# Kernel optimization log

Hardware: AMD Instinct MI355X
Metric: run time of the kernel (lower is better)

Reference implementation:

```python
import jax, jax.numpy as jnp
import numpy as np

EMB = 768
HEADS = 12
HEAD_DIM = EMB // HEADS
FF = 4 * EMB
EPS = 1e-5


def setup_inputs() -> dict:
    key = jax.random.key(0)
    ks = jax.random.split(key, 12)
    s = 0.02
    return {
        "x": jax.random.normal(ks[0], (4, 2048, EMB), dtype=jnp.float32),
        "ln1_scale": jnp.ones((EMB,), jnp.float32),
        "ln1_shift": jnp.zeros((EMB,), jnp.float32),
        # weights stored [in, out] (transpose of torch Linear layout)
        "wq": jax.random.normal(ks[1], (EMB, EMB), jnp.float32) * s,
        "wk": jax.random.normal(ks[2], (EMB, EMB), jnp.float32) * s,
        "wv": jax.random.normal(ks[3], (EMB, EMB), jnp.float32) * s,
        "wo": jax.random.normal(ks[4], (EMB, EMB), jnp.float32) * s,
        "bo": jnp.zeros((EMB,), jnp.float32),
        "ln2_scale": jnp.ones((EMB,), jnp.float32),
        "ln2_shift": jnp.zeros((EMB,), jnp.float32),
        "w1": jax.random.normal(ks[5], (EMB, FF), jnp.float32) * s,
        "b1": jnp.zeros((FF,), jnp.float32),
        "w2": jax.random.normal(ks[6], (FF, EMB), jnp.float32) * s,
        "b2": jnp.zeros((EMB,), jnp.float32),
    }


def _layernorm(x, scale, shift):
    mean = jnp.mean(x, axis=-1, keepdims=True)
    var = jnp.mean(jnp.square(x - mean), axis=-1, keepdims=True)  # unbiased=False
    return scale * (x - mean) / jnp.sqrt(var + EPS) + shift


def _gelu_tanh(x):
    c = jnp.sqrt(jnp.float32(2.0 / np.pi))
    return 0.5 * x * (1.0 + jnp.tanh(c * (x + 0.044715 * x * x * x)))


def _attention(x, wq, wk, wv, wo, bo):
    b, s, _ = x.shape
    q = (x @ wq).reshape(b, s, HEADS, HEAD_DIM).transpose(0, 2, 1, 3)
    k = (x @ wk).reshape(b, s, HEADS, HEAD_DIM).transpose(0, 2, 1, 3)
    v = (x @ wv).reshape(b, s, HEADS, HEAD_DIM).transpose(0, 2, 1, 3)
    scores = jnp.einsum("bhqd,bhkd->bhqk", q, k)  # [B,H,S,S]
    causal = jnp.tril(jnp.ones((s, s), dtype=bool))
    scores = jnp.where(causal, scores, -jnp.inf)
    weights = jax.nn.softmax(scores / jnp.sqrt(jnp.float32(HEAD_DIM)), axis=-1)
    ctx = jnp.einsum("bhqk,bhkd->bhqd", weights, v)
    ctx = ctx.transpose(0, 2, 1, 3).reshape(b, s, EMB)
    return ctx @ wo + bo


def reference(x, ln1_scale, ln1_shift, wq, wk, wv, wo, bo,
              ln2_scale, ln2_shift, w1, b1, w2, b2):
    # dropout rate is 0.0 (inference) -> identity
    x = x + _attention(_layernorm(x, ln1_scale, ln1_shift), wq, wk, wv, wo, bo)
    h = _layernorm(x, ln2_scale, ln2_shift)
    h = _gelu_tanh(h @ w1 + b1) @ w2 + b2
    return x + h
```

## Files before the change

kernel.cpp:

```cpp
#include <hip/hip_runtime.h>
#include <stdint.h>

#define EMB 768
#define SEQ 2048
#define BATCH 4
#define NHEADS 12
#define HDIM 64
#define FFDIM 3072
#define NTOK (BATCH*SEQ)
#define LNEPS 1e-5f
#define QSCALE 0.1803368801111137f

typedef __attribute__((ext_vector_type(8))) short bf16x8;
typedef __attribute__((ext_vector_type(4))) float f32x4;

__device__ __forceinline__ uint16_t f2bf(float f){
  union { float f; uint32_t u; } v; v.f = f;
  uint32_t r = v.u + 0x7fffu + ((v.u >> 16) & 1u);
  return (uint16_t)(r >> 16);
}
__device__ __forceinline__ uint32_t pk_rhu(float lo, float hi){
  union { float f; uint32_t u; } a, b; a.f = lo; b.f = hi;
  return __builtin_amdgcn_perm(b.u + 0x8000u, a.u + 0x8000u, 0x07060302u);
}

typedef __attribute__((address_space(3))) uint32_t lds32_t;
typedef __attribute__((address_space(1))) const uint32_t glb32_t;
__device__ __forceinline__ void gload16(const void* g, void* l){
  __builtin_amdgcn_global_load_lds((glb32_t*)(uintptr_t)g,
                                   (lds32_t*)(uintptr_t)l, 16, 0, 0);
}

struct TPtrs { const float* src[6]; uint16_t* dst[6]; };
__global__ __launch_bounds__(256) void transpose_all(TPtrs tp){
  int idx = blockIdx.x;
  int which, bx, by, K, N;
  if (idx < 2304){ which = idx/576; int l = idx - which*576; bx = l%24; by = l/24; K = 768;  N = 768;  }
  else if (idx < 4608){ which = 4; int l = idx-2304; bx = l%96; by = l/96; K = 768;  N = 3072; }
  else { which = 5; int l = idx-4608; bx = l%24; by = l/24; K = 3072; N = 768;  }
  const float* w = tp.src[which];
  uint16_t* wt   = tp.dst[which];
  __shared__ uint16_t tile[32][33];
  int n0 = bx*32, k0 = by*32;
  #pragma unroll
  for (int i=0;i<4;i++){
    int k = threadIdx.y + i*8;
    tile[k][threadIdx.x] = f2bf(w[(size_t)(k0+k)*N + n0 + threadIdx.x]);
  }
  __syncthreads();
  #pragma unroll
  for (int i=0;i<4;i++){
    int n = threadIdx.y + i*8;
    wt[(size_t)(n0+n)*K + k0 + threadIdx.x] = tile[threadIdx.x][n];
  }
}

__global__ __launch_bounds__(256) void ln_kernel(const float* __restrict__ x,
    const float* __restrict__ sc, const float* __restrict__ sh,
    uint16_t* __restrict__ out)
{
  int row = blockIdx.x*4 + (threadIdx.x>>6);
  int ln = threadIdx.x & 63;
  const float4* xr = (const float4*)(x + (size_t)row*EMB);
  float4 v0 = xr[ln], v1 = xr[64+ln], v2 = xr[128+ln];
  float s  = v0.x+v0.y+v0.z+v0.w + v1.x+v1.y+v1.z+v1.w + v2.x+v2.y+v2.z+v2.w;
  float s2 = v0.x*v0.x+v0.y*v0.y+v0.z*v0.z+v0.w*v0.w
           + v1.x*v1.x+v1.y*v1.y+v1.z*v1.z+v1.w*v1.w
           + v2.x*v2.x+v2.y*v2.y+v2.z*v2.z+v2.w*v2.w;
  #pragma unroll
  for (int off=1;off<64;off<<=1){ s += __shfl_xor(s,off); s2 += __shfl_xor(s2,off); }
  float mean = s*(1.f/768.f);
  float var  = s2*(1.f/768.f) - mean*mean;
  float rstd = rsqrtf(var + LNEPS);
  uint16_t* orow = out + (size_t)row*EMB;
  float4 vv[3] = {v0,v1,v2};
  #pragma unroll
  for (int i=0;i<3;i++){
    int c = (i*64+ln)*4;
    ushort4 o4;
    o4.x = f2bf((vv[i].x-mean)*rstd*sc[c+0] + sh[c+0]);
    o4.y = f2bf((vv[i].y-mean)*rstd*sc[c+1] + sh[c+1]);
    o4.z = f2bf((vv[i].z-mean)*rstd*sc[c+2] + sh[c+2]);
    o4.w = f2bf((vv[i].w-mean)*rstd*sc[c+3] + sh[c+3]);
    *(ushort4*)(orow + c) = o4;
  }
}

template<int MODE>
__global__ __launch_bounds__(256) void gemm_bt(const uint16_t* __restrict__ A,
    const uint16_t* __restrict__ Bt0,
    const float* __restrict__ bias,
    const float* __restrict__ resid,
    void* __restrict__ outp,
    uint16_t* __restrict__ vt_out,
    int N, int K, long bt_zstride, long out_zstride)
{
  __shared__ __align__(16) uint16_t As[128][32];
  __shared__ __align__(16) uint16_t Bs[128][32];
  const uint16_t* Bt = Bt0 + (size_t)blockIdx.z * bt_zstride;
  int tid = threadIdx.x;
  int wave = tid>>6, ln = tid&63, lane16 = ln&15, quad = ln>>4;
  int m0 = blockIdx.x*128, n0 = blockIdx.y*128;
  int wm = (wave>>1)*64, wn = (wave&1)*64;
  f32x4 zf = {0.f,0.f,0.f,0.f};
  f32x4 acc[4][4];
  #pragma unroll
  for (int i=0;i<4;i++)
    #pragma unroll
    for (int j=0;j<4;j++) acc[i][j]=zf;
  int ar = tid>>2;
  int ac = (tid&3)*8;
  const uint16_t* Arow0 = A  + (size_t)(m0+ar)*K    + ac;
  const uint16_t* Arow1 = A  + (size_t)(m0+ar+64)*K + ac;
  const uint16_t* Brow0 = Bt + (size_t)(n0+ar)*K    + ac;
  const uint16_t* Brow1 = Bt + (size_t)(n0+ar+64)*K + ac;
  char* lA = (char*)&As[0][0] + wave*1024;
  char* lB = (char*)&Bs[0][0] + wave*1024;
  for (int k0=0;k0<K;k0+=32){
    __syncthreads();
    gload16(Arow0 + k0, lA);
    gload16(Arow1 + k0, lA + 4096);
    gload16(Brow0 + k0, lB);
    gload16(Brow1 + k0, lB + 4096);
    __syncthreads();
    bf16x8 af[4], bfr[4];
    #pragma unroll
    for (int mi=0;mi<4;mi++) af[mi]  = *(const bf16x8*)&As[wm+mi*16+lane16][quad*8];
    #pragma unroll
    for (int ni=0;ni<4;ni++) bfr[ni] = *(const bf16x8*)&Bs[wn+ni*16+lane16][quad*8];
    #pragma unroll
    for (int mi=0;mi<4;mi++)
      #pragma unroll
      for (int ni=0;ni<4;ni++)
        acc[mi][ni] = __builtin_amdgcn_mfma_f32_16x16x32_bf16(af[mi], bfr[ni], acc[mi][ni], 0,0,0);
  }
  if (MODE==0 && blockIdx.z==2){
    #pragma unroll
    for (int mi=0;mi<4;mi++){
      int mrow0 = m0 + wm + mi*16 + quad*4;
      int bb = mrow0 >> 11, s = mrow0 & 2047;
      #pragma unroll
      for (int ni=0;ni<4;ni++){
        int ncol = n0 + wn + ni*16 + lane16;
        int hh = ncol >> 6, dd = ncol & 63;
        ushort4 o4 = { f2bf(acc[mi][ni][0]), f2bf(acc[mi][ni][1]),
                       f2bf(acc[mi][ni][2]), f2bf(acc[mi][ni][3]) };
        *(ushort4*)(vt_out + ((size_t)((bb*NHEADS+hh)*HDIM + dd))*SEQ + s) = o4;
      }
    }
    return;
  }
  float oscale = (MODE==0 && blockIdx.z==0) ? QSCALE : 1.0f;
  #pragma unroll
  for (int mi=0;mi<4;mi++){
    #pragma unroll
    for (int r=0;r<4;r++){
      int mrow = m0 + wm + mi*16 + quad*4 + r;
      #pragma unroll
      for (int ni=0;ni<4;ni++){
        int ncol = n0 + wn + ni*16 + lane16;
        float vv = acc[mi][ni][r];
        size_t idx = (size_t)mrow*N + ncol;
        if (MODE==0){
          ((uint16_t*)outp)[(size_t)blockIdx.z*out_zstride + idx] = f2bf(vv*oscale);
        } else if (MODE==1){
          ((float*)outp)[idx] = vv + bias[ncol] + resid[idx];
        } else if (MODE==2){
          float t = vv + bias[ncol];
          float u = 1.5957691216057308f*(t + 0.044715f*t*t*t);
          ((uint16_t*)outp)[idx] = f2bf(t / (1.f + __expf(-u)));
        } else {
          ((float*)outp)[idx] = vv + bias[ncol] + resid[idx];
        }
      }
    }
  }
}

__global__ __launch_bounds__(256, 3) void attn_kernel(const uint16_t* __restrict__ q,
    const uint16_t* __restrict__ k, const uint16_t* __restrict__ vt,
    uint16_t* __restrict__ ctx)
{
  __shared__ __align__(16) uint16_t Ks[2][8][64][8];
  __shared__ __align__(16) uint16_t Vs[2][8][64][8];
  const f32x4 zf = {0.f,0.f,0.f,0.f};
  int tid = threadIdx.x;
  int wave = tid>>6, ln = tid&63, l16 = ln&15, quad = ln>>4;
  int b = blockIdx.z, h = blockIdx.y;
  int p = blockIdx.x;
  size_t kgbase = ((size_t)(b*SEQ + ln))*EMB + h*HDIM;
  size_t vgbase = ((size_t)((b*NHEADS + h)*HDIM + ln))*SEQ;

  f32x4 o[4];
  float m_l, l_l;
  bf16x8 qf0, qf1;
  int q0w, myq;

  auto stage = [&](int buf, int kv0){
    #pragma unroll
    for (int i=0;i<2;i++){
      int c = wave + 4*i;
      gload16(k  + kgbase + (size_t)kv0*EMB + c*8, &Ks[buf][c][0][0]);
      gload16(vt + vgbase + kv0 + c*8,             &Vs[buf][c][0][0]);
    }
  };
  auto init_tile = [&](int tile){
    q0w = tile*64 + wave*16;
    myq = q0w + l16;
    const uint16_t* qrow = q + ((size_t)(b*SEQ + q0w + l16))*EMB + h*HDIM + quad*8;
    qf0 = *(const bf16x8*)(qrow);
    qf1 = *(const bf16x8*)(qrow + 32);
    o[0]=zf; o[1]=zf; o[2]=zf; o[3]=zf;
    m_l = -3.0e38f; l_l = 0.f;
  };
  auto writeout = [&](){
    float inv = 1.0f / l_l;
    uint16_t* crow = ctx + ((size_t)(b*SEQ + q0w + l16))*EMB + h*HDIM + quad*4;
    #pragma unroll
    for (int t=0; t<4; t++){
      ushort4 w4 = { f2bf(o[t][0]*inv), f2bf(o[t][1]*inv),
                     f2bf(o[t][2]*inv), f2bf(o[t][3]*inv) };
      *(ushort4*)(crow + t*16) = w4;
    }
  };
  auto compute = [&](int buf, int kv0, bool masked){
    bf16x8 kf[4][2], vf[2][4];
    #pragma unroll
    for (int f=0; f<4; f++){
      kf[f][0] = *(const bf16x8*)&Ks[buf][quad  ][f*16+l16][0];
      kf[f][1] = *(const bf16x8*)&Ks[buf][quad+4][f*16+l16][0];
    }
    #pragma unroll
    for (int t=0; t<4; t++){
      vf[0][t] = *(const bf16x8*)&Vs[buf][quad  ][t*16+l16][0];
      vf[1][t] = *(const bf16x8*)&Vs[buf][quad+4][t*16+l16][0];
    }
    f32x4 st[4];
    #pragma unroll
    for (int f=0; f<4; f++){
      st[f] = __builtin_amdgcn_mfma_f32_16x16x32_bf16(kf[f][0], qf0, zf, 0,0,0);
      st[f] = __builtin_amdgcn_mfma_f32_16x16x32_bf16(kf[f][1], qf1, st[f], 0,0,0);
    }
    if (masked){
      #pragma unroll
      for (int f=0; f<4; f++){
        int kvf = kv0 + f*16 + quad*4;
        #pragma unroll
        for (int r=0; r<4; r++)
          if (kvf + r > myq) st[f][r] = -1e30f;
      }
    }
    float cmax = -1e30f;
    #pragma unroll
    for (int f=0; f<4; f++)
      #pragma unroll
      for (int r=0; r<4; r++) cmax = fmaxf(cmax, st[f][r]);
    cmax = fmaxf(cmax, __shfl_xor(cmax,16));
    cmax = fmaxf(cmax, __shfl_xor(cmax,32));
    float mn = fmaxf(m_l, cmax);
    float alpha = __builtin_amdgcn_exp2f(m_l - mn);
    float rs = 0.f;
    #pragma unroll
    for (int f=0; f<4; f++)
      #pragma unroll
      for (int r=0; r<4; r++){
        st[f][r] = __builtin_amdgcn_exp2f(st[f][r] - mn);
        rs += st[f][r];
      }
    rs += __shfl_xor(rs,16); rs += __shfl_xor(rs,32);
    l_l = l_l*alpha + rs; m_l = mn;
    #pragma unroll
    for (int t=0; t<4; t++)
      #pragma unroll
      for (int r=0; r<4; r++) o[t][r] *= alpha;
    uint32_t dw[4][2];
    #pragma unroll
    for (int f=0; f<4; f++){
      dw[f][0] = pk_rhu(st[f][0], st[f][1]);
      dw[f][1] = pk_rhu(st[f][2], st[f][3]);
    }
    union { uint32_t u[4]; bf16x8 v; } pb[2];
    #pragma unroll
    for (int g=0; g<2; g++)
      #pragma unroll
      for (int j=0; j<4; j++){
        int src = 16*(2*(quad&1) + (j>>1)) + l16;
        uint32_t lo = (uint32_t)__shfl((int)dw[2*g  ][j&1], src, 64);
        uint32_t hi = (uint32_t)__shfl((int)dw[2*g+1][j&1], src, 64);
        pb[g].u[j] = (quad>>1) ? hi : lo;
      }
    #pragma unroll
    for (int t=0; t<4; t++){
      o[t] = __builtin_amdgcn_mfma_f32_16x16x32_bf16(vf[0][t], pb[0].v, o[t], 0,0,0);
      o[t] = __builtin_amdgcn_mfma_f32_16x16x32_bf16(vf[1][t], pb[1].v, o[t], 0,0,0);
    }
  };

  int n0 = p + 1, ntot = 33;
  init_tile(p);
  stage(0, 0);
  for (int s=0; s<ntot; s++){
    int sl = (s < n0) ? s : s - n0;
    int kv0 = sl*64;
    __syncthreads();
    if (s+1 < ntot){
      int sn = s+1;
      int snl = (sn < n0) ? sn : sn - n0;
      stage(sn&1, snl*64);
    }
    if (s == n0){ writeout(); init_tile(31 - p); }
    bool masked = (s == n0-1) || (s == ntot-1);
    compute(s&1, kv0, masked);
  }
  writeout();
}

extern "C" void kernel_launch(void* const* d_in, const int* in_sizes, int n_in,
                              void* d_out, int out_size, void* d_ws, size_t ws_size,
                              hipStream_t stream) {
  const float* x     = (const float*)d_in[0];
  const float* ln1_s = (const float*)d_in[1];
  const float* ln1_b = (const float*)d_in[2];
  const float* wq    = (const float*)d_in[3];
  const float* wk    = (const float*)d_in[4];
  const float* wv    = (const float*)d_in[5];
  const float* wo    = (const float*)d_in[6];
  const float* bo    = (const float*)d_in[7];
  const float* ln2_s = (const float*)d_in[8];
  const float* ln2_b = (const float*)d_in[9];
  const float* w1    = (const float*)d_in[10];
  const float* b1    = (const float*)d_in[11];
  const float* w2    = (const float*)d_in[12];
  const float* b2    = (const float*)d_in[13];

  uint16_t* wqkv_t = (uint16_t*)d_ws;
  uint16_t* wo_t   = wqkv_t + 3*EMB*EMB;
  uint16_t* w1_t   = wo_t   + EMB*EMB;
  uint16_t* w2_t   = w1_t   + (size_t)FFDIM*EMB;
  uint16_t* xn     = w2_t   + (size_t)EMB*FFDIM;
  uint16_t* qkv    = xn     + (size_t)NTOK*EMB;
  uint16_t* ctx    = qkv    + (size_t)3*NTOK*EMB;
  uint16_t* hff    = qkv;
  float*    x1     = (float*)(ctx + (size_t)NTOK*EMB);
  uint16_t* vt     = (uint16_t*)(x1 + (size_t)NTOK*EMB);

  TPtrs tp;
  tp.src[0]=wq; tp.src[1]=wk; tp.src[2]=wv; tp.src[3]=wo; tp.src[4]=w1; tp.src[5]=w2;
  tp.dst[0]=wqkv_t; tp.dst[1]=wqkv_t+EMB*EMB; tp.dst[2]=wqkv_t+2*EMB*EMB;
  tp.dst[3]=wo_t; tp.dst[4]=w1_t; tp.dst[5]=w2_t;
  transpose_all<<<6912, dim3(32,8), 0, stream>>>(tp);

  ln_kernel<<<NTOK/4, 256, 0, stream>>>(x, ln1_s, ln1_b, xn);
  gemm_bt<0><<<dim3(NTOK/128, EMB/128, 3), 256, 0, stream>>>(
      xn, wqkv_t, nullptr, nullptr, qkv, vt, EMB, EMB,
      (long)EMB*EMB, (long)NTOK*EMB);
  attn_kernel<<<dim3(16, NHEADS, BATCH), 256, 0, stream>>>(
      qkv, qkv + (size_t)NTOK*EMB, vt, ctx);
  gemm_bt<1><<<dim3(NTOK/128, EMB/128, 1), 256, 0, stream>>>(
      ctx, wo_t, bo, x, x1, nullptr, EMB, EMB, 0, 0);
  ln_kernel<<<NTOK/4, 256, 0, stream>>>(x1, ln2_s, ln2_b, xn);
  gemm_bt<2><<<dim3(NTOK/128, FFDIM/128, 1), 256, 0, stream>>>(
      xn, w1_t, b1, nullptr, hff, nullptr, FFDIM, EMB, 0, 0);
  gemm_bt<3><<<dim3(NTOK/128, EMB/128, 1), 256, 0, stream>>>(
      hff, w2_t, b2, x1, d_out, nullptr, EMB, FFDIM, 0, 0);
}
```

Measured before the change: 414.6 us.

## Double-buffer GEMM LDS tiles and use 64-row tiles for narrow-N GEMMs

The GEMM kernel gets two LDS buffers, so the next K-slice is fetched into one buffer while MFMAs run on the other. This removes one barrier per iteration and overlaps global-to-LDS loads with compute. A TM template parameter lets the N=768 output projection and FFN-down GEMMs use 64-row tiles, doubling their block count from 384 to 768 to fill the GPU better. Launch bounds now request 4 blocks per CU, which doubles LDS per block and may constrain registers.

```diff
diff --git a/kernel.cpp b/kernel.cpp
--- a/kernel.cpp
+++ b/kernel.cpp
@@ -86,8 +86,8 @@
   }
 }
 
-template<int MODE>
-__global__ __launch_bounds__(256) void gemm_bt(const uint16_t* __restrict__ A,
+template<int MODE, int TM>
+__global__ __launch_bounds__(256, 4) void gemm_bt(const uint16_t* __restrict__ A,
     const uint16_t* __restrict__ Bt0,
     const float* __restrict__ bias,
     const float* __restrict__ resid,
@@ -95,17 +95,18 @@
     uint16_t* __restrict__ vt_out,
     int N, int K, long bt_zstride, long out_zstride)
 {
-  __shared__ __align__(16) uint16_t As[128][32];
-  __shared__ __align__(16) uint16_t Bs[128][32];
+  constexpr int MI = TM/32;
+  __shared__ __align__(16) uint16_t As[2][TM][32];
+  __shared__ __align__(16) uint16_t Bs[2][128][32];
   const uint16_t* Bt = Bt0 + (size_t)blockIdx.z * bt_zstride;
   int tid = threadIdx.x;
   int wave = tid>>6, ln = tid&63, lane16 = ln&15, quad = ln>>4;
-  int m0 = blockIdx.x*128, n0 = blockIdx.y*128;
-  int wm = (wave>>1)*64, wn = (wave&1)*64;
+  int m0 = blockIdx.x*TM, n0 = blockIdx.y*128;
+  int wm = (wave>>1)*(MI*16), wn = (wave&1)*64;
   f32x4 zf = {0.f,0.f,0.f,0.f};
-  f32x4 acc[4][4];
-  #pragma unroll
-  for (int i=0;i<4;i++)
+  f32x4 acc[MI][4];
+  #pragma unroll
+  for (int i=0;i<MI;i++)
     #pragma unroll
     for (int j=0;j<4;j++) acc[i][j]=zf;
   int ar = tid>>2;
@@ -114,29 +115,36 @@
   const uint16_t* Arow1 = A  + (size_t)(m0+ar+64)*K + ac;
   const uint16_t* Brow0 = Bt + (size_t)(n0+ar)*K    + ac;
   const uint16_t* Brow1 = Bt + (size_t)(n0+ar+64)*K + ac;
-  char* lA = (char*)&As[0][0] + wave*1024;
-  char* lB = (char*)&Bs[0][0] + wave*1024;
-  for (int k0=0;k0<K;k0+=32){
-    __syncthreads();
+
+  auto stage = [&](int buf, int k0){
+    char* lA = (char*)&As[buf][0][0] + wave*1024;
+    char* lB = (char*)&Bs[buf][0][0] + wave*1024;
     gload16(Arow0 + k0, lA);
-    gload16(Arow1 + k0, lA + 4096);
+    if (TM==128) gload16(Arow1 + k0, lA + 4096);
     gload16(Brow0 + k0, lB);
     gload16(Brow1 + k0, lB + 4096);
+  };
+
+  int niter = K>>5;
+  stage(0, 0);
+  for (int s=0; s<niter; s++){
     __syncthreads();
-    bf16x8 af[4], bfr[4];
-    #pragma unroll
-    for (int mi=0;mi<4;mi++) af[mi]  = *(const bf16x8*)&As[wm+mi*16+lane16][quad*8];
-    #pragma unroll
-    for (int ni=0;ni<4;ni++) bfr[ni] = *(const bf16x8*)&Bs[wn+ni*16+lane16][quad*8];
-    #pragma unroll
-    for (int mi=0;mi<4;mi++)
+    if (s+1 < niter) stage((s+1)&1, (s+1)<<5);
+    int buf = s&1;
+    bf16x8 af[MI], bfr[4];
+    #pragma unroll
+    for (int mi=0;mi<MI;mi++) af[mi]  = *(const bf16x8*)&As[buf][wm+mi*16+lane16][quad*8];
+    #pragma unroll
+    for (int ni=0;ni<4;ni++)  bfr[ni] = *(const bf16x8*)&Bs[buf][wn+ni*16+lane16][quad*8];
+    #pragma unroll
+    for (int mi=0;mi<MI;mi++)
       #pragma unroll
       for (int ni=0;ni<4;ni++)
         acc[mi][ni] = __builtin_amdgcn_mfma_f32_16x16x32_bf16(af[mi], bfr[ni], acc[mi][ni], 0,0,0);
   }
   if (MODE==0 && blockIdx.z==2){
     #pragma unroll
-    for (int mi=0;mi<4;mi++){
+    for (int mi=0;mi<MI;mi++){
       int mrow0 = m0 + wm + mi*16 + quad*4;
       int bb = mrow0 >> 11, s = mrow0 & 2047;
       #pragma unroll
@@ -152,7 +160,7 @@
   }
   float oscale = (MODE==0 && blockIdx.z==0) ? QSCALE : 1.0f;
   #pragma unroll
-  for (int mi=0;mi<4;mi++){
+  for (int mi=0;mi<MI;mi++){
     #pragma unroll
     for (int r=0;r<4;r++){
       int mrow = m0 + wm + mi*16 + quad*4 + r;
@@ -351,16 +359,16 @@
   transpose_all<<<6912, dim3(32,8), 0, stream>>>(tp);
 
   ln_kernel<<<NTOK/4, 256, 0, stream>>>(x, ln1_s, ln1_b, xn);
-  gemm_bt<0><<<dim3(NTOK/128, EMB/128, 3), 256, 0, stream>>>(
+  gemm_bt<0,128><<<dim3(NTOK/128, EMB/128, 3), 256, 0, stream>>>(
       xn, wqkv_t, nullptr, nullptr, qkv, vt, EMB, EMB,
       (long)EMB*EMB, (long)NTOK*EMB);
   attn_kernel<<<dim3(16, NHEADS, BATCH), 256, 0, stream>>>(
       qkv, qkv + (size_t)NTOK*EMB, vt, ctx);
-  gemm_bt<1><<<dim3(NTOK/128, EMB/128, 1), 256, 0, stream>>>(
+  gemm_bt<1,64><<<dim3(NTOK/64, EMB/128, 1), 256, 0, stream>>>(
       ctx, wo_t, bo, x, x1, nullptr, EMB, EMB, 0, 0);
   ln_kernel<<<NTOK/4, 256, 0, stream>>>(x1, ln2_s, ln2_b, xn);
-  gemm_bt<2><<<dim3(NTOK/128, FFDIM/128, 1), 256, 0, stream>>>(
+  gemm_bt<2,128><<<dim3(NTOK/128, FFDIM/128, 1), 256, 0, stream>>>(
       xn, w1_t, b1, nullptr, hff, nullptr, FFDIM, EMB, 0, 0);
-  gemm_bt<3><<<dim3(NTOK/128, EMB/128, 1), 256, 0, stream>>>(
+  gemm_bt<3,64><<<dim3(NTOK/64, EMB/128, 1), 256, 0, stream>>>(
       hff, w2_t, b2, x1, d_out, nullptr, EMB, FFDIM, 0, 0);
 }
```

After: 380.9 us. -8.1%, faster.
